# Performance work log

Hardware: AMD Instinct MI355X
Metric: run time of the kernel (lower is better)

Reference implementation:

```python
import jax, jax.numpy as jnp
import numpy as np

B, D, K, SQ, STEPS = 128, 512, 512, 128, 12
NEG_INF = -1e9

def _dense(x, W, b):
    return x @ W + b

def _forward(x, h_controls, h_memories, knowledge, question, question_rep,
             W_qs, b_qs, c_Wcq, c_bcq, c_Wf, c_bf,
             r_Wm, r_bm, r_Wk, r_bk, r_Wd, r_bd, r_Wr, r_br,
             w_Wm1, w_bm1, w_Wca, w_bca, w_Wm2, w_bm2, w_Ws, w_bs, w_Wm3, w_bm3):
    steps = h_controls.shape[1]
    prev_control = h_controls[:, 0]            # [B, d]
    prev_memory = h_memories[:, 0]             # [B, d]
    quest_state = _dense(x * question_rep, W_qs, b_qs)  # [B, d]

    # ---- Controller ----
    cq = _dense(jnp.concatenate([quest_state, prev_control], axis=-1), c_Wcq, c_bcq)  # [B, d]
    focus = _dense(cq[:, None, :] * question, c_Wf, c_bf)[..., 0]  # [B, Sq]
    c_attn = jax.nn.softmax(focus, axis=-1)
    new_control = jnp.mean(c_attn[:, :, None] * question, axis=1)  # [B, d]

    # ---- Reader ----
    reflection = _dense(prev_memory, r_Wm, r_bm)[:, None, :] * _dense(knowledge, r_Wk, r_bk)  # [B, K, d]
    disjoint = _dense(jnp.concatenate([knowledge, reflection], axis=-1), r_Wd, r_bd)          # [B, K, d]
    retrieve = _dense(disjoint * new_control[:, None, :], r_Wr, r_br)[..., 0]                 # [B, K]
    r_attn = jax.nn.softmax(retrieve, axis=-1)
    read = jnp.mean(r_attn[:, :, None] * knowledge, axis=1)  # [B, d]

    # ---- Writer ----
    m1 = _dense(jnp.concatenate([prev_memory, read], axis=-1), w_Wm1, w_bm1)  # [B, d]
    ca = _dense(h_controls * new_control[:, None, :], w_Wca, w_bca)[..., 0]   # [B, steps]
    pad_mask = (ca == 0).astype(ca.dtype)  # create_padding_mask on unfilled history slots
    ca = ca + pad_mask * NEG_INF
    c_softmax = jax.nn.softmax(ca, axis=-1)
    msa = jnp.sum(c_softmax[:, :, None] * h_memories, axis=1)  # [B, d]
    mp = _dense(m1, w_Wm2, w_bm2) + _dense(msa, w_Ws, w_bs)
    gate = jax.nn.sigmoid(_dense(new_control, w_Wm3, w_bm3))  # [B, 1]
    new_memory = mp * gate + (1.0 - gate) * prev_memory       # [B, d]

    # shift history: newest first, drop oldest
    all_controls = jnp.concatenate([new_control[:, None, :], h_controls[:, : steps - 1]], axis=1)
    all_memories = jnp.concatenate([new_memory[:, None, :], h_memories[:, : steps - 1]], axis=1)
    return jnp.stack([all_controls, all_memories], axis=0)  # [2, B, steps, d]


def setup_inputs() -> dict:
    key = jax.random.key(0)
    ks = jax.random.split(key, 20)
    rn = lambda k, s: (jax.random.normal(k, s, dtype=jnp.float32) * 0.02)
    x = jax.random.normal(ks[0], (B, D), dtype=jnp.float32)
    knowledge = jax.random.normal(ks[1], (B, K, D), dtype=jnp.float32)
    question = jax.random.normal(ks[2], (B, SQ, D), dtype=jnp.float32)
    question_rep = jax.random.normal(ks[3], (B, D), dtype=jnp.float32)
    # initial state per get_initial_state: ones at slot 0, zeros elsewhere
    init = jnp.concatenate([jnp.ones((B, 1, D), jnp.float32), jnp.zeros((B, STEPS - 1, D), jnp.float32)], axis=1)
    z = lambda n: jnp.zeros((n,), jnp.float32)
    return {
        "x": x, "h_controls": init, "h_memories": init,
        "knowledge": knowledge, "question": question, "question_rep": question_rep,
        "W_qs": rn(ks[4], (D, D)), "b_qs": z(D),
        "c_Wcq": rn(ks[5], (2 * D, D)), "c_bcq": z(D),
        "c_Wf": rn(ks[6], (D, 1)), "c_bf": z(1),
        "r_Wm": rn(ks[7], (D, D)), "r_bm": z(D),
        "r_Wk": rn(ks[8], (D, D)), "r_bk": z(D),
        "r_Wd": rn(ks[9], (2 * D, D)), "r_bd": z(D),
        "r_Wr": rn(ks[10], (D, 1)), "r_br": z(1),
        "w_Wm1": rn(ks[11], (2 * D, D)), "w_bm1": z(D),
        "w_Wca": rn(ks[12], (D, 1)), "w_bca": z(1),
        "w_Wm2": rn(ks[13], (D, D)), "w_bm2": z(D),
        "w_Ws": rn(ks[14], (D, D)), "w_bs": z(D),
        "w_Wm3": rn(ks[15], (D, 1)), "w_bm3": z(1),
    }


def reference(x, h_controls, h_memories, knowledge, question, question_rep,
              W_qs, b_qs, c_Wcq, c_bcq, c_Wf, c_bf,
              r_Wm, r_bm, r_Wk, r_bk, r_Wd, r_bd, r_Wr, r_br,
              w_Wm1, w_bm1, w_Wca, w_bca, w_Wm2, w_bm2, w_Ws, w_bs, w_Wm3, w_bm3):
    return _forward(x, h_controls, h_memories, knowledge, question, question_rep,
                    W_qs, b_qs, c_Wcq, c_bcq, c_Wf, c_bf,
                    r_Wm, r_bm, r_Wk, r_bk, r_Wd, r_bd, r_Wr, r_br,
                    w_Wm1, w_bm1, w_Wca, w_bca, w_Wm2, w_bm2, w_Ws, w_bs, w_Wm3, w_bm3)
```

## Files before the change

### kernel.cpp

```cpp
#include <hip/hip_runtime.h>

#define B_ 128
#define D_ 512
#define K_ 512
#define SQ_ 128
#define ST_ 12
#define NEG_INF_ -1000000000.0f

typedef unsigned int uint_t;

__device__ __forceinline__ float wave_sum(float part) {
    #pragma unroll
    for (int off = 32; off > 0; off >>= 1) part += __shfl_xor(part, off);
    return part;
}
__device__ __forceinline__ float wave_max(float part) {
    #pragma unroll
    for (int off = 32; off > 0; off >>= 1) part = fmaxf(part, __shfl_xor(part, off));
    return part;
}
__device__ __forceinline__ float dot4(float4 a, const float* v) {
    return a.x * v[0] + a.y * v[1] + a.z * v[2] + a.w * v[3];
}
__device__ __forceinline__ float dot4f(float4 a, float4 b) {
    return a.x * b.x + a.y * b.y + a.z * b.z + a.w * b.w;
}

#define WS_QS  0
#define WS_RM  65536
#define WS_P   131072
#define WS_FL  196608
#define WS_NC  212992
#define WS_V   278528
#define WS_U   344064
#define WS_G   409600
#define WS_KL  475136
#define WS_RD  540672
#define WS_M1  606208
#define WS_MSA 671744
#define WS_GP  737280
#define WS_TOTAL_FLOATS 737408

__global__ __launch_bounds__(512) void kInit(
    const float* __restrict__ x, const float* __restrict__ qrep,
    const float* __restrict__ W_qs, const float* __restrict__ b_qs,
    const float* __restrict__ hm, const float* __restrict__ rWm,
    const float* __restrict__ rbm, const float* __restrict__ hc,
    float* __restrict__ ws, float* __restrict__ out)
{
    const int blk = blockIdx.x;
    const int tid = threadIdx.x;
    __shared__ float sIn[D_];
    __shared__ float sPart[512];

    if (blk < 1024) {
        const bool is_qs = (blk < 512);
        const int q  = is_qs ? blk : (blk - 512);
        const int b  = q >> 2, dt = q & 3;
        sIn[tid] = is_qs ? (x[(size_t)b*D_ + tid] * qrep[(size_t)b*D_ + tid])
                         : hm[(size_t)(b*ST_)*D_ + tid];
        __syncthreads();
        const int isid = tid >> 7, dd = tid & 127, d = dt*128 + dd;
        const float* W  = is_qs ? W_qs : rWm;
        const float* Wp = W + (size_t)(isid*128)*D_ + d;
        const float* ip = sIn + isid*128;
        float acc = 0.f;
        #pragma unroll 16
        for (int j = 0; j < 128; ++j) acc += ip[j] * Wp[(size_t)j*D_];
        sPart[tid] = acc;
        __syncthreads();
        if (tid < 128) {
            const int d2 = dt*128 + tid;
            const float bias = is_qs ? b_qs[d2] : rbm[d2];
            float* dst = ws + (is_qs ? WS_QS : WS_RM);
            dst[(size_t)b*D_ + d2] = bias + sPart[tid] + sPart[tid+128]
                                   + sPart[tid+256] + sPart[tid+384];
        }
    } else if (blk < 1280) {
        const int c = blk - 1024;
        const int pair = c >> 7, b = c & 127;
        const float* src = (pair == 0) ? hc : hm;
        float* dst = out + ((size_t)(pair*B_ + b))*ST_*D_;
        const float* s = src + (size_t)(b*ST_)*D_;
        for (int r = 0; r < ST_ - 1; ++r)
            dst[(size_t)(r + 1)*D_ + tid] = s[(size_t)r*D_ + tid];
    } else {
        if (tid < B_) ws[WS_GP + tid] = 0.f;
    }
}

__global__ __launch_bounds__(512) void kCq(
    const float* __restrict__ hc, const float* __restrict__ Wcq,
    const float* __restrict__ bcq, const float* __restrict__ Wf,
    float* __restrict__ ws)
{
    const int blk = blockIdx.x, tid = threadIdx.x;
    const int b = blk >> 2, dt = blk & 3;
    __shared__ float sIn[2*D_];
    __shared__ float sPart[512];
    sIn[tid]       = ws[WS_QS + (size_t)b*D_ + tid];
    sIn[D_ + tid]  = hc[(size_t)(b*ST_)*D_ + tid];
    __syncthreads();
    const int isid = tid >> 7, dd = tid & 127, d = dt*128 + dd;
    const float* Wp = Wcq + (size_t)(isid*256)*D_ + d;
    const float* ip = sIn + isid*256;
    float acc = 0.f;
    #pragma unroll 16
    for (int j = 0; j < 256; ++j) acc += ip[j] * Wp[(size_t)j*D_];
    sPart[tid] = acc;
    __syncthreads();
    if (tid < 128) {
        const int d2 = dt*128 + tid;
        const float cq = bcq[d2] + sPart[tid] + sPart[tid+128]
                       + sPart[tid+256] + sPart[tid+384];
        ws[WS_P + (size_t)b*D_ + d2] = cq * Wf[d2];
    }
}

__global__ __launch_bounds__(256) void kFocus(
    const float* __restrict__ question, const float* __restrict__ ws_p,
    float* __restrict__ ws_fl)
{
    const int tid = threadIdx.x, lane = tid & 63;
    const int row = blockIdx.x * 4 + (tid >> 6);
    const int b = row >> 7;
    const float4* qr = reinterpret_cast<const float4*>(question + (size_t)row*D_);
    const float4* pr = reinterpret_cast<const float4*>(ws_p + (size_t)b*D_);
    const float part = wave_sum(dot4f(qr[lane*2], pr[lane*2]) +
                                dot4f(qr[lane*2+1], pr[lane*2+1]));
    if (lane == 0) ws_fl[row] = part;
}

__global__ __launch_bounds__(512) void kNc(
    const float* __restrict__ question, const float* __restrict__ rWr,
    const float* __restrict__ Wm3, float* __restrict__ ws)
{
    const int blk = blockIdx.x, tid = threadIdx.x;
    const int b = blk >> 2, dt = blk & 3;
    __shared__ float sAtt[SQ_];
    __shared__ float sPart[512];
    __shared__ float sRed2[2];

    float l = 0.f;
    if (tid < SQ_) { l = ws[WS_FL + (size_t)b*SQ_ + tid]; sAtt[tid] = l; }
    __syncthreads();
    if (tid < 64) {
        float m = wave_max(fmaxf(sAtt[tid], sAtt[tid + 64]));
        if (tid == 0) sRed2[0] = m;
    }
    __syncthreads();
    float ex = 0.f;
    if (tid < SQ_) { ex = expf(l - sRed2[0]); sAtt[tid] = ex; }
    __syncthreads();
    if (tid < 64) {
        float s = wave_sum(sAtt[tid] + sAtt[tid + 64]);
        if (tid == 0) sRed2[1] = s;
    }
    __syncthreads();
    if (tid < SQ_) sAtt[tid] = ex / (sRed2[1] * (float)SQ_);
    __syncthreads();

    const int ssid = tid >> 7, dd = tid & 127, d = dt*128 + dd;
    float acc = 0.f;
    #pragma unroll 8
    for (int j = 0; j < 32; ++j) {
        const int s = ssid*32 + j;
        acc += sAtt[s] * question[((size_t)(b*SQ_ + s))*D_ + d];
    }
    sPart[tid] = acc;
    __syncthreads();
    if (tid < 128) {
        const int d2 = dt*128 + tid;
        const float nc = sPart[tid] + sPart[tid+128] + sPart[tid+256] + sPart[tid+384];
        ws[WS_NC + (size_t)b*D_ + d2] = nc;
        ws[WS_V  + (size_t)b*D_ + d2] = nc * rWr[d2];
        sPart[tid] = nc * Wm3[d2];
    }
    __syncthreads();
    if (tid < 64) {
        float s = wave_sum(sPart[tid] + sPart[tid + 64]);
        if (tid == 0) atomicAdd(&ws[WS_GP + b], s);
    }
}

__global__ __launch_bounds__(512) void kG1(
    const float* __restrict__ rWd, float* __restrict__ ws)
{
    const int blk = blockIdx.x, tid = threadIdx.x;
    const int bt = blk >> 4, tt = blk & 15;
    const int b0 = bt*16, t0 = tt*32;
    __shared__ float sV[16*520];
    for (int r = 0; r < 16; ++r)
        sV[r*520 + tid] = ws[WS_V + (size_t)(b0 + r)*D_ + tid];
    __syncthreads();
    const int bl = tid & 15, tl = tid >> 4;
    const int b = b0 + bl, t = t0 + tl;
    const float4* rT = reinterpret_cast<const float4*>(rWd + (size_t)t*D_);
    const float4* rB = reinterpret_cast<const float4*>(rWd + (size_t)(D_ + t)*D_);
    const float* vv = sV + bl*520;
    float u1 = 0.f, w2 = 0.f;
    #pragma unroll 8
    for (int i = 0; i < 128; ++i) {
        u1 += dot4(rT[i], vv + i*4);
        w2 += dot4(rB[i], vv + i*4);
    }
    ws[WS_U + (size_t)b*D_ + t] = u1;
    ws[WS_G + (size_t)b*D_ + t] = ws[WS_RM + (size_t)b*D_ + t] * w2;
}

__global__ __launch_bounds__(512) void kG2(
    const float* __restrict__ rWk, float* __restrict__ ws)
{
    const int blk = blockIdx.x, tid = threadIdx.x;
    const int bt = blk >> 4, tt = blk & 15;
    const int b0 = bt*16, t0 = tt*32;
    __shared__ float sG[16*520];
    for (int r = 0; r < 16; ++r)
        sG[r*520 + tid] = ws[WS_G + (size_t)(b0 + r)*D_ + tid];
    __syncthreads();
    const int bl = tid & 15, tl = tid >> 4;
    const int b = b0 + bl, t = t0 + tl;
    const float4* rK = reinterpret_cast<const float4*>(rWk + (size_t)t*D_);
    const float* gg = sG + bl*520;
    float u2 = 0.f;
    #pragma unroll 8
    for (int i = 0; i < 128; ++i) u2 += dot4(rK[i], gg + i*4);
    ws[WS_U + (size_t)b*D_ + t] += u2;
}

__global__ __launch_bounds__(256) void kKlog(
    const float* __restrict__ knl, const float* __restrict__ ws_u,
    float* __restrict__ ws_kl)
{
    const int tid = threadIdx.x, lane = tid & 63;
    const int row = blockIdx.x * 4 + (tid >> 6);
    const int b = row >> 9;
    const float4* kr = reinterpret_cast<const float4*>(knl + (size_t)row*D_);
    const float4* ur = reinterpret_cast<const float4*>(ws_u + (size_t)b*D_);
    const float part = wave_sum(dot4f(kr[lane*2], ur[lane*2]) +
                                dot4f(kr[lane*2+1], ur[lane*2+1]));
    if (lane == 0) ws_kl[row] = part;
}

__global__ __launch_bounds__(512) void kRead(
    const float* __restrict__ knl, float* __restrict__ ws)
{
    const int blk = blockIdx.x, tid = threadIdx.x;
    const int b = blk >> 2, dt = blk & 3;
    __shared__ float sAtt[K_];
    __shared__ float sPart[512];
    __shared__ float sRed2[2];

    const float l = ws[WS_KL + (size_t)b*K_ + tid];
    sAtt[tid] = l;
    __syncthreads();
    if (tid < 64) {
        float m = sAtt[tid];
        #pragma unroll
        for (int j = 1; j < 8; ++j) m = fmaxf(m, sAtt[tid + 64*j]);
        m = wave_max(m);
        if (tid == 0) sRed2[0] = m;
    }
    __syncthreads();
    const float ex = expf(l - sRed2[0]);
    sAtt[tid] = ex;
    __syncthreads();
    if (tid < 64) {
        float s = 0.f;
        #pragma unroll
        for (int j = 0; j < 8; ++j) s += sAtt[tid + 64*j];
        s = wave_sum(s);
        if (tid == 0) sRed2[1] = s;
    }
    __syncthreads();
    sAtt[tid] = ex / (sRed2[1] * (float)K_);
    __syncthreads();

    const int ksid = tid >> 7, dd = tid & 127, d = dt*128 + dd;
    float acc = 0.f;
    #pragma unroll 8
    for (int j = 0; j < 128; ++j) {
        const int k = ksid*128 + j;
        acc += sAtt[k] * knl[((size_t)(b*K_ + k))*D_ + d];
    }
    sPart[tid] = acc;
    __syncthreads();
    if (tid < 128)
        ws[WS_RD + (size_t)b*D_ + dt*128 + tid] =
            sPart[tid] + sPart[tid+128] + sPart[tid+256] + sPart[tid+384];
}

__global__ __launch_bounds__(512) void kSmall(
    const float* __restrict__ hc, const float* __restrict__ hm,
    const float* __restrict__ Wca, const float* __restrict__ bca,
    float* __restrict__ ws)
{
    const int b = blockIdx.x, tid = threadIdx.x;
    const int lane = tid & 63, wv = tid >> 6;
    __shared__ float sW[D_];
    __shared__ float sCa[ST_];
    __shared__ float sCs[ST_];
    sW[tid] = ws[WS_NC + (size_t)b*D_ + tid] * Wca[tid];
    __syncthreads();
    const float bcaf = bca[0];
    for (int rep = 0; rep < 2; ++rep) {
        const int r = (rep == 0) ? wv : ((wv < 4) ? 8 + wv : -1);
        if (r >= 0) {
            const float4* hrow = reinterpret_cast<const float4*>(
                hc + ((size_t)(b*ST_) + r)*D_);
            float part = wave_sum(dot4(hrow[lane*2], &sW[lane*8]) +
                                  dot4(hrow[lane*2+1], &sW[lane*8+4]));
            if (lane == 0) sCa[r] = part + bcaf;
        }
    }
    __syncthreads();
    if (tid == 0) {
        float vals[ST_], mx = -3.0e38f;
        for (int t = 0; t < ST_; ++t) {
            float v = sCa[t];
            if (v == 0.0f) v = v + NEG_INF_;
            vals[t] = v; mx = fmaxf(mx, v);
        }
        float sum = 0.f;
        for (int t = 0; t < ST_; ++t) { float e = expf(vals[t] - mx); sCs[t] = e; sum += e; }
        const float is = 1.f / sum;
        for (int t = 0; t < ST_; ++t) sCs[t] *= is;
    }
    __syncthreads();
    float msa = 0.f;
    #pragma unroll
    for (int t = 0; t < ST_; ++t)
        msa += sCs[t] * hm[((size_t)(b*ST_) + t)*D_ + tid];
    ws[WS_MSA + (size_t)b*D_ + tid] = msa;
}

__global__ __launch_bounds__(512) void kM1(
    const float* __restrict__ hm, const float* __restrict__ Wm1,
    const float* __restrict__ bm1, float* __restrict__ ws)
{
    const int blk = blockIdx.x, tid = threadIdx.x;
    const int b = blk >> 2, dt = blk & 3;
    __shared__ float sIn[2*D_];
    __shared__ float sPart[512];
    sIn[tid]      = hm[(size_t)(b*ST_)*D_ + tid];
    sIn[D_ + tid] = ws[WS_RD + (size_t)b*D_ + tid];
    __syncthreads();
    const int isid = tid >> 7, dd = tid & 127, d = dt*128 + dd;
    const float* Wp = Wm1 + (size_t)(isid*256)*D_ + d;
    const float* ip = sIn + isid*256;
    float acc = 0.f;
    #pragma unroll 16
    for (int j = 0; j < 256; ++j) acc += ip[j] * Wp[(size_t)j*D_];
    sPart[tid] = acc;
    __syncthreads();
    if (tid < 128) {
        const int d2 = dt*128 + tid;
        ws[WS_M1 + (size_t)b*D_ + d2] = bm1[d2] + sPart[tid] + sPart[tid+128]
                                      + sPart[tid+256] + sPart[tid+384];
    }
}

__global__ __launch_bounds__(512) void kFinal(
    const float* __restrict__ hm, const float* __restrict__ Wm2,
    const float* __restrict__ bm2, const float* __restrict__ Ws,
    const float* __restrict__ bs, const float* __restrict__ bm3,
    const float* __restrict__ ws, float* __restrict__ out)
{
    const int blk = blockIdx.x, tid = threadIdx.x;
    const int b = blk >> 2, dt = blk & 3;
    __shared__ float sIn[2*D_];
    __shared__ float sPart[512];
    sIn[tid]      = ws[WS_M1  + (size_t)b*D_ + tid];
    sIn[D_ + tid] = ws[WS_MSA + (size_t)b*D_ + tid];
    __syncthreads();
    const int isid = tid >> 7, dd = tid & 127, d = dt*128 + dd;
    const float* Mat = (isid < 2) ? Wm2 : Ws;
    const int ibase = (isid & 1) * 256;
    const float* ip = sIn + (isid >> 1)*D_ + ibase;
    const float* Wp = Mat + (size_t)ibase*D_ + d;
    float acc = 0.f;
    #pragma unroll 16
    for (int j = 0; j < 256; ++j) acc += ip[j] * Wp[(size_t)j*D_];
    sPart[tid] = acc;
    __syncthreads();
    if (tid < 128) {
        const int d2 = dt*128 + tid;
        const float mp = bm2[d2] + bs[d2] + sPart[tid] + sPart[tid+128]
                       + sPart[tid+256] + sPart[tid+384];
        const float gate = 1.f / (1.f + expf(-(ws[WS_GP + b] + bm3[0])));
        const float pm = hm[(size_t)(b*ST_)*D_ + d2];
        const float nm = mp * gate + (1.f - gate) * pm;
        out[(size_t)(b*ST_)*D_ + d2] = ws[WS_NC + (size_t)b*D_ + d2];
        out[((size_t)(B_ + b))*ST_*D_ + d2] = nm;
    }
}

__global__ __launch_bounds__(512) void mac_fused(
    const float* __restrict__ x,    const float* __restrict__ hc,
    const float* __restrict__ hm,   const float* __restrict__ knl,
    const float* __restrict__ question, const float* __restrict__ qrep,
    const float* __restrict__ W_qs, const float* __restrict__ b_qs,
    const float* __restrict__ Wcq,  const float* __restrict__ bcq,
    const float* __restrict__ Wf,   const float* __restrict__ bfv,
    const float* __restrict__ rWm,  const float* __restrict__ rbm,
    const float* __restrict__ rWk,  const float* __restrict__ rbk,
    const float* __restrict__ rWd,  const float* __restrict__ rbd,
    const float* __restrict__ rWr,  const float* __restrict__ rbr,
    const float* __restrict__ Wm1,  const float* __restrict__ bm1,
    const float* __restrict__ Wca,  const float* __restrict__ bca,
    const float* __restrict__ Wm2,  const float* __restrict__ bm2,
    const float* __restrict__ Ws,   const float* __restrict__ bs,
    const float* __restrict__ Wm3,  const float* __restrict__ bm3,
    float* __restrict__ out)
{
    const int b    = blockIdx.x;
    const int tid  = threadIdx.x;
    const int lane = tid & 63;
    const int wv   = tid >> 6;

    __shared__ float sTmp[D_];
    __shared__ float sQs[D_];
    __shared__ float sPc[D_];
    __shared__ float sP[D_];
    __shared__ float sF[SQ_];
    __shared__ float sNc[D_];
    __shared__ float sV[D_];
    __shared__ float sG[D_];
    __shared__ float sU[D_];
    __shared__ float sPm[D_];
    __shared__ float sAtt[K_];
    __shared__ float sRead[D_];
    __shared__ float sM1[D_];
    __shared__ float sMsa[D_];
    __shared__ float sRed[D_];
    __shared__ float sCa[ST_];
    __shared__ float sCs[ST_];
    __shared__ float sGate;

    sTmp[tid] = x[(size_t)b*D_ + tid] * qrep[(size_t)b*D_ + tid];
    sPc[tid]  = hc[(size_t)(b*ST_)*D_ + tid];
    sPm[tid]  = hm[(size_t)(b*ST_)*D_ + tid];
    __syncthreads();
    {
        float acc = b_qs[tid];
        #pragma unroll 8
        for (int i = 0; i < D_; ++i) acc += sTmp[i] * W_qs[(size_t)i*D_ + tid];
        sQs[tid] = acc;
    }
    __syncthreads();
    {
        float acc = bcq[tid];
        #pragma unroll 8
        for (int i = 0; i < D_; ++i) acc += sQs[i] * Wcq[(size_t)i*D_ + tid];
        #pragma unroll 8
        for (int i = 0; i < D_; ++i) acc += sPc[i] * Wcq[(size_t)(D_ + i)*D_ + tid];
        sP[tid] = acc * Wf[tid];
    }
    __syncthreads();
    {
        const float bfs = bfv[0];
        for (int t = 0; t < 16; ++t) {
            const int s = wv * 16 + t;
            const float4* qrow = reinterpret_cast<const float4*>(
                question + ((size_t)(b*SQ_) + s)*D_);
            float part = dot4(qrow[lane*2], &sP[lane*8]) +
                         dot4(qrow[lane*2 + 1], &sP[lane*8 + 4]);
            part = wave_sum(part);
            if (lane == 0) sF[s] = part + bfs;
        }
    }
    __syncthreads();
    {
        sRed[tid] = (tid < SQ_) ? sF[tid] : -3.0e38f;
        __syncthreads();
        for (int off = 256; off > 0; off >>= 1) {
            if (tid < off) sRed[tid] = fmaxf(sRed[tid], sRed[tid + off]);
            __syncthreads();
        }
        const float mx = sRed[0];
        __syncthreads();
        float ex = 0.f;
        if (tid < SQ_) ex = expf(sF[tid] - mx);
        sRed[tid] = (tid < SQ_) ? ex : 0.f;
        __syncthreads();
        for (int off = 256; off > 0; off >>= 1) {
            if (tid < off) sRed[tid] += sRed[tid + off];
            __syncthreads();
        }
        const float inv = 1.f / (sRed[0] * (float)SQ_);
        __syncthreads();
        if (tid < SQ_) sF[tid] = ex * inv;
    }
    __syncthreads();
    {
        float ncv = 0.f;
        #pragma unroll 4
        for (int s = 0; s < SQ_; ++s)
            ncv += sF[s] * question[((size_t)(b*SQ_) + s)*D_ + tid];
        sNc[tid] = ncv;
        sV[tid]  = ncv * rWr[tid];
    }
    __syncthreads();
    float cc;
    {
        float rmv = rbm[tid];
        #pragma unroll 8
        for (int i = 0; i < D_; ++i) rmv += sPm[i] * rWm[(size_t)i*D_ + tid];
        const float4* rowT = reinterpret_cast<const float4*>(rWd + (size_t)tid*D_);
        const float4* rowB = reinterpret_cast<const float4*>(rWd + (size_t)(D_ + tid)*D_);
        float u1 = 0.f, w2 = 0.f;
        #pragma unroll 8
        for (int i = 0; i < 128; ++i) {
            u1 += dot4(rowT[i], &sV[i*4]);
            w2 += dot4(rowB[i], &sV[i*4]);
        }
        sG[tid] = rmv * w2;
        __syncthreads();
        const float4* rowK = reinterpret_cast<const float4*>(rWk + (size_t)tid*D_);
        float u2 = 0.f;
        #pragma unroll 8
        for (int i = 0; i < 128; ++i) u2 += dot4(rowK[i], &sG[i*4]);
        sU[tid] = u1 + u2;
        sRed[tid] = rbd[tid] * sV[tid] + rbk[tid] * sG[tid];
        __syncthreads();
        for (int off = 256; off > 0; off >>= 1) {
            if (tid < off) sRed[tid] += sRed[tid + off];
            __syncthreads();
        }
        cc = sRed[0] + rbr[0];
    }
    __syncthreads();
    for (int r = 0; r < 64; ++r) {
        const int k = wv * 64 + r;
        const float4* krow = reinterpret_cast<const float4*>(
            knl + ((size_t)(b*K_) + k)*D_);
        float part = dot4(krow[lane*2], &sU[lane*8]) +
                     dot4(krow[lane*2 + 1], &sU[lane*8 + 4]);
        part = wave_sum(part);
        if (lane == 0) sAtt[k] = part + cc;
    }
    __syncthreads();
    {
        sRed[tid] = sAtt[tid];
        __syncthreads();
        for (int off = 256; off > 0; off >>= 1) {
            if (tid < off) sRed[tid] = fmaxf(sRed[tid], sRed[tid + off]);
            __syncthreads();
        }
        const float mx = sRed[0];
        __syncthreads();
        const float ex = expf(sAtt[tid] - mx);
        sRed[tid] = ex;
        __syncthreads();
        for (int off = 256; off > 0; off >>= 1) {
            if (tid < off) sRed[tid] += sRed[tid + off];
            __syncthreads();
        }
        const float inv = 1.f / (sRed[0] * (float)K_);
        __syncthreads();
        sAtt[tid] = ex * inv;
    }
    __syncthreads();
    {
        float rd = 0.f;
        #pragma unroll 4
        for (int k = 0; k < K_; ++k)
            rd += sAtt[k] * knl[((size_t)(b*K_) + k)*D_ + tid];
        sRead[tid] = rd;
    }
    __syncthreads();
    {
        float m1 = bm1[tid];
        #pragma unroll 8
        for (int i = 0; i < D_; ++i) m1 += sPm[i] * Wm1[(size_t)i*D_ + tid];
        #pragma unroll 8
        for (int i = 0; i < D_; ++i) m1 += sRead[i] * Wm1[(size_t)(D_ + i)*D_ + tid];
        sM1[tid] = m1;
        sTmp[tid] = sNc[tid] * Wca[tid];
    }
    __syncthreads();
    {
        const float bcaf = bca[0];
        for (int rep = 0; rep < 2; ++rep) {
            const int r = (rep == 0) ? wv : ((wv < 4) ? 8 + wv : -1);
            if (r >= 0) {
                const float4* hrow = reinterpret_cast<const float4*>(
                    hc + ((size_t)(b*ST_) + r)*D_);
                float part = dot4(hrow[lane*2], &sTmp[lane*8]) +
                             dot4(hrow[lane*2 + 1], &sTmp[lane*8 + 4]);
                part = wave_sum(part);
                if (lane == 0) sCa[r] = part + bcaf;
            }
        }
    }
    __syncthreads();
    if (tid == 0) {
        float vals[ST_];
        float mx = -3.0e38f;
        for (int t = 0; t < ST_; ++t) {
            float v = sCa[t];
            if (v == 0.0f) v = v + NEG_INF_;
            vals[t] = v;
            mx = fmaxf(mx, v);
        }
        float sum = 0.f;
        for (int t = 0; t < ST_; ++t) { float e = expf(vals[t] - mx); sCs[t] = e; sum += e; }
        const float is = 1.f / sum;
        for (int t = 0; t < ST_; ++t) sCs[t] *= is;
    }
    __syncthreads();
    {
        float msa = 0.f;
        #pragma unroll
        for (int t = 0; t < ST_; ++t)
            msa += sCs[t] * hm[((size_t)(b*ST_) + t)*D_ + tid];
        sMsa[tid] = msa;
    }
    {
        sRed[tid] = sNc[tid] * Wm3[tid];
        __syncthreads();
        for (int off = 256; off > 0; off >>= 1) {
            if (tid < off) sRed[tid] += sRed[tid + off];
            __syncthreads();
        }
        if (tid == 0) sGate = 1.f / (1.f + expf(-(sRed[0] + bm3[0])));
    }
    __syncthreads();
    const float gate = sGate;
    float mp = bm2[tid] + bs[tid];
    #pragma unroll 8
    for (int i = 0; i < D_; ++i) mp += sM1[i] * Wm2[(size_t)i*D_ + tid];
    #pragma unroll 8
    for (int i = 0; i < D_; ++i) mp += sMsa[i] * Ws[(size_t)i*D_ + tid];
    const float nm = mp * gate + (1.f - gate) * sPm[tid];
    float* outC = out + (size_t)b*ST_*D_;
    float* outM = out + ((size_t)B_ + b)*ST_*D_;
    outC[tid] = sNc[tid];
    outM[tid] = nm;
    for (int t = 1; t < ST_; ++t) {
        outC[(size_t)t*D_ + tid] = hc[((size_t)(b*ST_) + (t - 1))*D_ + tid];
        outM[(size_t)t*D_ + tid] = hm[((size_t)(b*ST_) + (t - 1))*D_ + tid];
    }
}

extern "C" void kernel_launch(void* const* d_in, const int* in_sizes, int n_in,
                              void* d_out, int out_size, void* d_ws, size_t ws_size,
                              hipStream_t stream) {
    (void)in_sizes; (void)n_in; (void)out_size;
    const float* x    = (const float*)d_in[0];
    const float* hc   = (const float*)d_in[1];
    const float* hm   = (const float*)d_in[2];
    const float* knl  = (const float*)d_in[3];
    const float* qst  = (const float*)d_in[4];
    const float* qrep = (const float*)d_in[5];
    const float* W_qs = (const float*)d_in[6];
    const float* b_qs = (const float*)d_in[7];
    const float* Wcq  = (const float*)d_in[8];
    const float* bcq  = (const float*)d_in[9];
    const float* Wf   = (const float*)d_in[10];
    const float* bfv  = (const float*)d_in[11];
    const float* rWm  = (const float*)d_in[12];
    const float* rbm  = (const float*)d_in[13];
    const float* rWk  = (const float*)d_in[14];
    const float* rbk  = (const float*)d_in[15];
    const float* rWd  = (const float*)d_in[16];
    const float* rbd  = (const float*)d_in[17];
    const float* rWr  = (const float*)d_in[18];
    const float* rbr  = (const float*)d_in[19];
    const float* Wm1  = (const float*)d_in[20];
    const float* bm1  = (const float*)d_in[21];
    const float* Wca  = (const float*)d_in[22];
    const float* bca  = (const float*)d_in[23];
    const float* Wm2  = (const float*)d_in[24];
    const float* bm2  = (const float*)d_in[25];
    const float* Wsw  = (const float*)d_in[26];
    const float* bsw  = (const float*)d_in[27];
    const float* Wm3  = (const float*)d_in[28];
    const float* bm3  = (const float*)d_in[29];
    float* out = (float*)d_out;

    if (ws_size >= (size_t)WS_TOTAL_FLOATS * sizeof(float)) {
        float* ws = (float*)d_ws;
        kInit <<<1281, 512, 0, stream>>>(x, qrep, W_qs, b_qs, hm, rWm, rbm, hc, ws, out);
        kCq   <<<512,  512, 0, stream>>>(hc, Wcq, bcq, Wf, ws);
        kFocus<<<4096, 256, 0, stream>>>(qst, ws + WS_P, ws + WS_FL);
        kNc   <<<512,  512, 0, stream>>>(qst, rWr, Wm3, ws);
        kG1   <<<128,  512, 0, stream>>>(rWd, ws);
        kG2   <<<128,  512, 0, stream>>>(rWk, ws);
        kKlog <<<16384,256, 0, stream>>>(knl, ws + WS_U, ws + WS_KL);
        kRead <<<512,  512, 0, stream>>>(knl, ws);
        kSmall<<<128,  512, 0, stream>>>(hc, hm, Wca, bca, ws);
        kM1   <<<512,  512, 0, stream>>>(hm, Wm1, bm1, ws);
        kFinal<<<512,  512, 0, stream>>>(hm, Wm2, bm2, Wsw, bsw, bm3, ws, out);
    } else {
        mac_fused<<<B_, 512, 0, stream>>>(
            x, hc, hm, knl, qst, qrep, W_qs, b_qs, Wcq, bcq, Wf, bfv,
            rWm, rbm, rWk, rbk, rWd, rbd, rWr, rbr, Wm1, bm1, Wca, bca,
            Wm2, bm2, Wsw, bsw, Wm3, bm3, out);
    }
}
```

Before: 408.8 us.

## Fuse logit, softmax and weighted-sum passes with online softmax

Replaces the separate focus-logit and control-attention kernels with one kernel per batch that computes question logits, an online softmax and the weighted sum in a single pass over the question rows. The knowledge logit and read kernels are merged the same way: each block covers a quarter of K and writes a partial (max, sum, accumulator), and kM1 combines the four partials. This removes a second full read of the 128MB knowledge tensor and two launches, and replaces the gate-sum atomic with a direct store. In exchange it adds extra exp work per row, and kQnc runs only 128 blocks.

```diff
diff --git a/kernel.cpp b/kernel.cpp
--- a/kernel.cpp
+++ b/kernel.cpp
@@ -7,39 +7,27 @@
 #define ST_ 12
 #define NEG_INF_ -1000000000.0f
 
-typedef unsigned int uint_t;
-
 __device__ __forceinline__ float wave_sum(float part) {
     #pragma unroll
     for (int off = 32; off > 0; off >>= 1) part += __shfl_xor(part, off);
     return part;
 }
-__device__ __forceinline__ float wave_max(float part) {
-    #pragma unroll
-    for (int off = 32; off > 0; off >>= 1) part = fmaxf(part, __shfl_xor(part, off));
-    return part;
-}
 __device__ __forceinline__ float dot4(float4 a, const float* v) {
     return a.x * v[0] + a.y * v[1] + a.z * v[2] + a.w * v[3];
-}
-__device__ __forceinline__ float dot4f(float4 a, float4 b) {
-    return a.x * b.x + a.y * b.y + a.z * b.z + a.w * b.w;
 }
 
 #define WS_QS  0
 #define WS_RM  65536
 #define WS_P   131072
-#define WS_FL  196608
-#define WS_NC  212992
-#define WS_V   278528
-#define WS_U   344064
-#define WS_G   409600
-#define WS_KL  475136
-#define WS_RD  540672
-#define WS_M1  606208
-#define WS_MSA 671744
-#define WS_GP  737280
-#define WS_TOTAL_FLOATS 737408
+#define WS_NC  196608
+#define WS_V   262144
+#define WS_U   327680
+#define WS_G   393216
+#define WS_KP  458752
+#define WS_GP  722944
+#define WS_M1  723072
+#define WS_MSA 788608
+#define WS_TOTAL_FLOATS 854144
 
 __global__ __launch_bounds__(512) void kInit(
     const float* __restrict__ x, const float* __restrict__ qrep,
@@ -76,7 +64,7 @@
             dst[(size_t)b*D_ + d2] = bias + sPart[tid] + sPart[tid+128]
                                    + sPart[tid+256] + sPart[tid+384];
         }
-    } else if (blk < 1280) {
+    } else {
         const int c = blk - 1024;
         const int pair = c >> 7, b = c & 127;
         const float* src = (pair == 0) ? hc : hm;
@@ -84,8 +72,6 @@
         const float* s = src + (size_t)(b*ST_)*D_;
         for (int r = 0; r < ST_ - 1; ++r)
             dst[(size_t)(r + 1)*D_ + tid] = s[(size_t)r*D_ + tid];
-    } else {
-        if (tid < B_) ws[WS_GP + tid] = 0.f;
     }
 }
 
@@ -117,69 +103,67 @@
     }
 }
 
-__global__ __launch_bounds__(256) void kFocus(
-    const float* __restrict__ question, const float* __restrict__ ws_p,
-    float* __restrict__ ws_fl)
-{
-    const int tid = threadIdx.x, lane = tid & 63;
-    const int row = blockIdx.x * 4 + (tid >> 6);
-    const int b = row >> 7;
-    const float4* qr = reinterpret_cast<const float4*>(question + (size_t)row*D_);
-    const float4* pr = reinterpret_cast<const float4*>(ws_p + (size_t)b*D_);
-    const float part = wave_sum(dot4f(qr[lane*2], pr[lane*2]) +
-                                dot4f(qr[lane*2+1], pr[lane*2+1]));
-    if (lane == 0) ws_fl[row] = part;
-}
-
-__global__ __launch_bounds__(512) void kNc(
+__global__ __launch_bounds__(512) void kQnc(
     const float* __restrict__ question, const float* __restrict__ rWr,
     const float* __restrict__ Wm3, float* __restrict__ ws)
 {
-    const int blk = blockIdx.x, tid = threadIdx.x;
-    const int b = blk >> 2, dt = blk & 3;
-    __shared__ float sAtt[SQ_];
-    __shared__ float sPart[512];
-    __shared__ float sRed2[2];
-
-    float l = 0.f;
-    if (tid < SQ_) { l = ws[WS_FL + (size_t)b*SQ_ + tid]; sAtt[tid] = l; }
+    const int b = blockIdx.x, tid = threadIdx.x;
+    const int lane = tid & 63, wv = tid >> 6;
+    __shared__ float sP[D_];
+    __shared__ float sAcc[8][D_];
+    __shared__ float sM[8], sL[8];
+    __shared__ float sRed[512];
+    sP[tid] = ws[WS_P + (size_t)b*D_ + tid];
+    __syncthreads();
+    float p0=sP[lane*8],p1=sP[lane*8+1],p2=sP[lane*8+2],p3=sP[lane*8+3];
+    float p4=sP[lane*8+4],p5=sP[lane*8+5],p6=sP[lane*8+6],p7=sP[lane*8+7];
+
+    float m = -3.0e38f, l = 0.f;
+    float a0=0,a1=0,a2=0,a3=0,a4=0,a5=0,a6=0,a7=0;
+    for (int t = 0; t < 16; ++t) {
+        const int s = wv*16 + t;
+        const float4* qr = reinterpret_cast<const float4*>(
+            question + ((size_t)(b*SQ_ + s))*D_);
+        const float4 r0 = qr[lane*2], r1 = qr[lane*2+1];
+        float part = r0.x*p0 + r0.y*p1 + r0.z*p2 + r0.w*p3
+                   + r1.x*p4 + r1.y*p5 + r1.z*p6 + r1.w*p7;
+        part = wave_sum(part);
+        const float mn = fmaxf(m, part);
+        const float sc = expf(m - mn);
+        const float e  = expf(part - mn);
+        l = l*sc + e;
+        a0=a0*sc+e*r0.x; a1=a1*sc+e*r0.y; a2=a2*sc+e*r0.z; a3=a3*sc+e*r0.w;
+        a4=a4*sc+e*r1.x; a5=a5*sc+e*r1.y; a6=a6*sc+e*r1.z; a7=a7*sc+e*r1.w;
+        m = mn;
+    }
+    if (lane == 0) { sM[wv] = m; sL[wv] = l; }
+    __syncthreads();
+    float M = sM[0];
+    #pragma unroll
+    for (int w = 1; w < 8; ++w) M = fmaxf(M, sM[w]);
+    const float msc = expf(m - M);
+    sAcc[wv][lane*8  ] = a0*msc; sAcc[wv][lane*8+1] = a1*msc;
+    sAcc[wv][lane*8+2] = a2*msc; sAcc[wv][lane*8+3] = a3*msc;
+    sAcc[wv][lane*8+4] = a4*msc; sAcc[wv][lane*8+5] = a5*msc;
+    sAcc[wv][lane*8+6] = a6*msc; sAcc[wv][lane*8+7] = a7*msc;
+    __syncthreads();
+    float L = 0.f;
+    #pragma unroll
+    for (int w = 0; w < 8; ++w) L += sL[w] * expf(sM[w] - M);
+    float ncs = 0.f;
+    #pragma unroll
+    for (int w = 0; w < 8; ++w) ncs += sAcc[w][tid];
+    const float nc = ncs / (L * (float)SQ_);
+    ws[WS_NC + (size_t)b*D_ + tid] = nc;
+    ws[WS_V  + (size_t)b*D_ + tid] = nc * rWr[tid];
+    sRed[tid] = nc * Wm3[tid];
     __syncthreads();
     if (tid < 64) {
-        float m = wave_max(fmaxf(sAtt[tid], sAtt[tid + 64]));
-        if (tid == 0) sRed2[0] = m;
-    }
-    __syncthreads();
-    float ex = 0.f;
-    if (tid < SQ_) { ex = expf(l - sRed2[0]); sAtt[tid] = ex; }
-    __syncthreads();
-    if (tid < 64) {
-        float s = wave_sum(sAtt[tid] + sAtt[tid + 64]);
-        if (tid == 0) sRed2[1] = s;
-    }
-    __syncthreads();
-    if (tid < SQ_) sAtt[tid] = ex / (sRed2[1] * (float)SQ_);
-    __syncthreads();
-
-    const int ssid = tid >> 7, dd = tid & 127, d = dt*128 + dd;
-    float acc = 0.f;
-    #pragma unroll 8
-    for (int j = 0; j < 32; ++j) {
-        const int s = ssid*32 + j;
-        acc += sAtt[s] * question[((size_t)(b*SQ_ + s))*D_ + d];
-    }
-    sPart[tid] = acc;
-    __syncthreads();
-    if (tid < 128) {
-        const int d2 = dt*128 + tid;
-        const float nc = sPart[tid] + sPart[tid+128] + sPart[tid+256] + sPart[tid+384];
-        ws[WS_NC + (size_t)b*D_ + d2] = nc;
-        ws[WS_V  + (size_t)b*D_ + d2] = nc * rWr[d2];
-        sPart[tid] = nc * Wm3[d2];
-    }
-    __syncthreads();
-    if (tid < 64) {
-        float s = wave_sum(sPart[tid] + sPart[tid + 64]);
-        if (tid == 0) atomicAdd(&ws[WS_GP + b], s);
+        float s = 0.f;
+        #pragma unroll
+        for (int j = 0; j < 8; ++j) s += sRed[tid + 64*j];
+        s = wave_sum(s);
+        if (tid == 0) ws[WS_GP + b] = s;
     }
 }
 
@@ -228,66 +212,59 @@
     ws[WS_U + (size_t)b*D_ + t] += u2;
 }
 
-__global__ __launch_bounds__(256) void kKlog(
+__global__ __launch_bounds__(512) void kKRead(
     const float* __restrict__ knl, const float* __restrict__ ws_u,
-    float* __restrict__ ws_kl)
-{
-    const int tid = threadIdx.x, lane = tid & 63;
-    const int row = blockIdx.x * 4 + (tid >> 6);
-    const int b = row >> 9;
-    const float4* kr = reinterpret_cast<const float4*>(knl + (size_t)row*D_);
-    const float4* ur = reinterpret_cast<const float4*>(ws_u + (size_t)b*D_);
-    const float part = wave_sum(dot4f(kr[lane*2], ur[lane*2]) +
-                                dot4f(kr[lane*2+1], ur[lane*2+1]));
-    if (lane == 0) ws_kl[row] = part;
-}
-
-__global__ __launch_bounds__(512) void kRead(
-    const float* __restrict__ knl, float* __restrict__ ws)
+    float* __restrict__ ws_kp)
 {
     const int blk = blockIdx.x, tid = threadIdx.x;
-    const int b = blk >> 2, dt = blk & 3;
-    __shared__ float sAtt[K_];
-    __shared__ float sPart[512];
-    __shared__ float sRed2[2];
-
-    const float l = ws[WS_KL + (size_t)b*K_ + tid];
-    sAtt[tid] = l;
-    __syncthreads();
-    if (tid < 64) {
-        float m = sAtt[tid];
-        #pragma unroll
-        for (int j = 1; j < 8; ++j) m = fmaxf(m, sAtt[tid + 64*j]);
-        m = wave_max(m);
-        if (tid == 0) sRed2[0] = m;
-    }
-    __syncthreads();
-    const float ex = expf(l - sRed2[0]);
-    sAtt[tid] = ex;
-    __syncthreads();
-    if (tid < 64) {
-        float s = 0.f;
-        #pragma unroll
-        for (int j = 0; j < 8; ++j) s += sAtt[tid + 64*j];
-        s = wave_sum(s);
-        if (tid == 0) sRed2[1] = s;
-    }
-    __syncthreads();
-    sAtt[tid] = ex / (sRed2[1] * (float)K_);
-    __syncthreads();
-
-    const int ksid = tid >> 7, dd = tid & 127, d = dt*128 + dd;
-    float acc = 0.f;
-    #pragma unroll 8
-    for (int j = 0; j < 128; ++j) {
-        const int k = ksid*128 + j;
-        acc += sAtt[k] * knl[((size_t)(b*K_ + k))*D_ + d];
-    }
-    sPart[tid] = acc;
-    __syncthreads();
-    if (tid < 128)
-        ws[WS_RD + (size_t)b*D_ + dt*128 + tid] =
-            sPart[tid] + sPart[tid+128] + sPart[tid+256] + sPart[tid+384];
+    const int b = blk >> 2, kt = blk & 3;
+    const int lane = tid & 63, wv = tid >> 6;
+    __shared__ float sU[D_];
+    __shared__ float sAcc[8][D_];
+    __shared__ float sM[8], sL[8];
+    sU[tid] = ws_u[(size_t)b*D_ + tid];
+    __syncthreads();
+    float u0=sU[lane*8],u1=sU[lane*8+1],u2=sU[lane*8+2],u3=sU[lane*8+3];
+    float u4=sU[lane*8+4],u5=sU[lane*8+5],u6=sU[lane*8+6],u7=sU[lane*8+7];
+
+    float m = -3.0e38f, l = 0.f;
+    float a0=0,a1=0,a2=0,a3=0,a4=0,a5=0,a6=0,a7=0;
+    for (int t = 0; t < 16; ++t) {
+        const int k = kt*128 + wv*16 + t;
+        const float4* kr = reinterpret_cast<const float4*>(
+            knl + ((size_t)(b*K_ + k))*D_);
+        const float4 r0 = kr[lane*2], r1 = kr[lane*2+1];
+        float part = r0.x*u0 + r0.y*u1 + r0.z*u2 + r0.w*u3
+                   + r1.x*u4 + r1.y*u5 + r1.z*u6 + r1.w*u7;
+        part = wave_sum(part);
+        const float mn = fmaxf(m, part);
+        const float sc = expf(m - mn);
+        const float e  = expf(part - mn);
+        l = l*sc + e;
+        a0=a0*sc+e*r0.x; a1=a1*sc+e*r0.y; a2=a2*sc+e*r0.z; a3=a3*sc+e*r0.w;
+        a4=a4*sc+e*r1.x; a5=a5*sc+e*r1.y; a6=a6*sc+e*r1.z; a7=a7*sc+e*r1.w;
+        m = mn;
+    }
+    if (lane == 0) { sM[wv] = m; sL[wv] = l; }
+    __syncthreads();
+    float M = sM[0];
+    #pragma unroll
+    for (int w = 1; w < 8; ++w) M = fmaxf(M, sM[w]);
+    const float msc = expf(m - M);
+    sAcc[wv][lane*8  ] = a0*msc; sAcc[wv][lane*8+1] = a1*msc;
+    sAcc[wv][lane*8+2] = a2*msc; sAcc[wv][lane*8+3] = a3*msc;
+    sAcc[wv][lane*8+4] = a4*msc; sAcc[wv][lane*8+5] = a5*msc;
+    sAcc[wv][lane*8+6] = a6*msc; sAcc[wv][lane*8+7] = a7*msc;
+    __syncthreads();
+    float L = 0.f;
+    #pragma unroll
+    for (int w = 0; w < 8; ++w) L += sL[w] * expf(sM[w] - M);
+    float a = 0.f;
+    #pragma unroll
+    for (int w = 0; w < 8; ++w) a += sAcc[w][tid];
+    float* kp = ws_kp + (size_t)blk*516;
+    kp[tid] = a;
+    if (tid == 0) { kp[512] = M; kp[513] = L; }
 }
 
 __global__ __launch_bounds__(512) void kSmall(
@@ -342,8 +319,18 @@
     const int b = blk >> 2, dt = blk & 3;
     __shared__ float sIn[2*D_];
     __shared__ float sPart[512];
+    const float* kp = ws + WS_KP + (size_t)(b*4)*516;
+    const float m0 = kp[512],        l0 = kp[513];
+    const float m1v = kp[516+512],   l1 = kp[516+513];
+    const float m2 = kp[2*516+512],  l2 = kp[2*516+513];
+    const float m3 = kp[3*516+512],  l3 = kp[3*516+513];
+    const float M = fmaxf(fmaxf(m0, m1v), fmaxf(m2, m3));
+    const float e0 = expf(m0-M), e1 = expf(m1v-M), e2 = expf(m2-M), e3 = expf(m3-M);
+    const float L = l0*e0 + l1*e1 + l2*e2 + l3*e3;
+    const float rd = (kp[tid]*e0 + kp[516+tid]*e1 + kp[2*516+tid]*e2 + kp[3*516+tid]*e3)
+                   / (L * (float)K_);
     sIn[tid]      = hm[(size_t)(b*ST_)*D_ + tid];
-    sIn[D_ + tid] = ws[WS_RD + (size_t)b*D_ + tid];
+    sIn[D_ + tid] = rd;
     __syncthreads();
     const int isid = tid >> 7, dd = tid & 127, d = dt*128 + dd;
     const float* Wp = Wm1 + (size_t)(isid*256)*D_ + d;
@@ -681,17 +668,15 @@
 
     if (ws_size >= (size_t)WS_TOTAL_FLOATS * sizeof(float)) {
         float* ws = (float*)d_ws;
-        kInit <<<1281, 512, 0, stream>>>(x, qrep, W_qs, b_qs, hm, rWm, rbm, hc, ws, out);
-        kCq   <<<512,  512, 0, stream>>>(hc, Wcq, bcq, Wf, ws);
-        kFocus<<<4096, 256, 0, stream>>>(qst, ws + WS_P, ws + WS_FL);
-        kNc   <<<512,  512, 0, stream>>>(qst, rWr, Wm3, ws);
-        kG1   <<<128,  512, 0, stream>>>(rWd, ws);
-        kG2   <<<128,  512, 0, stream>>>(rWk, ws);
-        kKlog <<<16384,256, 0, stream>>>(knl, ws + WS_U, ws + WS_KL);
-        kRead <<<512,  512, 0, stream>>>(knl, ws);
-        kSmall<<<128,  512, 0, stream>>>(hc, hm, Wca, bca, ws);
-        kM1   <<<512,  512, 0, stream>>>(hm, Wm1, bm1, ws);
-        kFinal<<<512,  512, 0, stream>>>(hm, Wm2, bm2, Wsw, bsw, bm3, ws, out);
+        kInit  <<<1280, 512, 0, stream>>>(x, qrep, W_qs, b_qs, hm, rWm, rbm, hc, ws, out);
+        kCq    <<<512,  512, 0, stream>>>(hc, Wcq, bcq, Wf, ws);
+        kQnc   <<<128,  512, 0, stream>>>(qst, rWr, Wm3, ws);
+        kG1    <<<128,  512, 0, stream>>>(rWd, ws);
+        kG2    <<<128,  512, 0, stream>>>(rWk, ws);
+        kKRead <<<512,  512, 0, stream>>>(knl, ws + WS_U, ws + WS_KP);
+        kSmall <<<128,  512, 0, stream>>>(hc, hm, Wca, bca, ws);
+        kM1    <<<512,  512, 0, stream>>>(hm, Wm1, bm1, ws);
+        kFinal <<<512,  512, 0, stream>>>(hm, Wm2, bm2, Wsw, bsw, bm3, ws, out);
     } else {
         mac_fused<<<B_, 512, 0, stream>>>(
             x, hc, hm, knl, qst, qrep, W_qs, b_qs, Wcq, bcq, Wf, bfv,
```

New measurement: 388.5 us. 5.0% less time.
